# Performance work log

Hardware: AMD Instinct MI355X
Metric: run time of the kernel (lower is better)

The kernel has to match this reference:

```python
import jax, jax.numpy as jnp
import numpy as np
from jax import lax


def _edt(mask):
    """Exact Euclidean distance transform: for boolean mask [B,H,W], return the
    distance from each True pixel to the nearest False pixel (0 on False pixels).
    Two-phase separable algorithm:
      phase 1: 1D distance along axis H (rows) via forward/backward scans.
      phase 2: D2[i,j] = min_j' ( g[i,j']^2 + (j-j')^2 ) along axis W.
    """
    B, H, W = mask.shape
    BIG = jnp.float32(H + W)  # cap: larger than any in-image distance
    mT = jnp.transpose(mask, (1, 0, 2))  # [H,B,W] for scanning over rows

    def step(carry, m_row):
        d = jnp.where(m_row, jnp.minimum(carry + 1.0, BIG), 0.0)
        return d, d

    init = jnp.full((B, W), BIG, dtype=jnp.float32)
    _, fwd = lax.scan(step, init, mT)          # dist to nearest False above
    _, bwd = lax.scan(step, init, mT[::-1])    # dist to nearest False below
    g = jnp.minimum(fwd, bwd[::-1])            # [H,B,W] exact 1D vertical distance
    g2 = g * g

    j = jnp.arange(W, dtype=jnp.float32)
    sq = (j[:, None] - j[None, :]) ** 2        # [W(j), W(j')]
    # D2[h,b,j] = min_j' g2[h,b,j'] + (j-j')^2   (intermediate [H,B,W,W])
    D2 = jnp.min(g2[..., None, :] + sq, axis=-1)
    return jnp.sqrt(D2).transpose(1, 0, 2)     # [B,H,W]


def _dt(z):
    """Faithful port of the torch `dt`: fg-EDT + bg-EDT, zero if no foreground."""
    fg = z > 0.5
    f_dist = _edt(fg)        # distance from foreground pixels to background
    b_dist = _edt(~fg)       # distance from background pixels to foreground
    has_fg = jnp.any(fg, axis=(1, 2))[:, None, None]
    return jnp.where(has_fg, f_dist + b_dist, 0.0)


def setup_inputs() -> dict:
    key = jax.random.key(0)
    kx, ky = jax.random.split(key)
    x = jax.random.uniform(kx, (8, 256, 256), dtype=jnp.float32)
    y = jax.random.uniform(ky, (8, 256, 256), dtype=jnp.float32)
    return {"x": x, "y": y}


def reference(x, y):
    # distance transforms are computed on detached tensors in the original
    dt_x = lax.stop_gradient(_dt(x))
    dt_y = lax.stop_gradient(_dt(y))
    err = (x - y) ** 2
    dist = dt_x ** 2 + dt_y ** 2
    return jnp.mean(err * dist)
```

## Files before the change

kernel.cpp:

```cpp
#include <hip/hip_runtime.h>

#define BB 8
#define HH 256
#define WW 256
#define BHW (BB*HH*WW)
#define BIGV 512.0f


__global__ __launch_bounds__(256) void edt_vert(const float* __restrict__ x,
                                                const float* __restrict__ y,
                                                unsigned short* __restrict__ gdist,
                                                int* __restrict__ blkflag) {
    __shared__ float Cf[2][16][16];
    __shared__ float Cb[2][16][16];
    __shared__ int sAny;

    int blk = blockIdx.x;
    int tileIdx = blk & 15;
    int b  = (blk >> 4) & 7;
    int ip = blk >> 7;
    int t = threadIdx.x;
    int c = t & 15, s = t >> 4;

    if (t == 0) sAny = 0;

    const float* src = (ip ? y : x) + (size_t)b*HH*WW + tileIdx*16 + c;

    unsigned m = 0;
    const float* p = src + (size_t)(s*16)*WW;
    #pragma unroll
    for (int i = 0; i < 16; ++i) {
        if (p[(size_t)i*WW] > 0.5f) m |= (1u << i);
    }

    unsigned invm = (~m) & 0xFFFFu;
    Cf[0][s][c] = invm ? (float)(15 - (31 - __clz((int)invm))) : 1e9f;
    Cb[0][s][c] = invm ? (float)(__ffs((int)invm) - 1)          : 1e9f;
    Cf[1][s][c] = m    ? (float)(15 - (31 - __clz((int)m)))     : 1e9f;
    Cb[1][s][c] = m    ? (float)(__ffs((int)m) - 1)             : 1e9f;
    __syncthreads();
    if (m) sAny = 1;

    float e0 = BIGV, e1 = BIGV;
    #pragma unroll
    for (int sp = 0; sp < 15; ++sp) {
        float c0 = Cf[0][sp][c], c1 = Cf[1][sp][c];
        bool act = sp < s;
        e0 = act ? fminf(fminf(e0 + 16.0f, BIGV), c0) : e0;
        e1 = act ? fminf(fminf(e1 + 16.0f, BIGV), c1) : e1;
    }
    float f0 = BIGV, f1 = BIGV;
    #pragma unroll
    for (int sp = 15; sp >= 1; --sp) {
        float c0 = Cb[0][sp][c], c1 = Cb[1][sp][c];
        bool act = sp > s;
        f0 = act ? fminf(fminf(f0 + 16.0f, BIGV), c0) : f0;
        f1 = act ? fminf(fminf(f1 + 16.0f, BIGV), c1) : f1;
    }

    float b0v[16], b1v[16];
    float d0 = f0, d1 = f1;
    #pragma unroll
    for (int i = 15; i >= 0; --i) {
        bool bit = (m >> i) & 1u;
        d0 = !bit ? 0.0f : fminf(d0 + 1.0f, BIGV);
        d1 =  bit ? 0.0f : fminf(d1 + 1.0f, BIGV);
        b0v[i] = d0; b1v[i] = d1;
    }
    size_t base = (size_t)(ip*BB + b)*HH*WW + tileIdx*16 + c;
    d0 = e0; d1 = e1;
    #pragma unroll
    for (int i = 0; i < 16; ++i) {
        bool bit = (m >> i) & 1u;
        d0 = !bit ? 0.0f : fminf(d0 + 1.0f, BIGV);
        d1 =  bit ? 0.0f : fminf(d1 + 1.0f, BIGV);
        float g0 = fminf(d0, b0v[i]);
        float g1 = fminf(d1, b1v[i]);
        float gs = bit ? g0 : g1;
        gdist[base + (size_t)(s*16 + i)*WW] = (unsigned short)(int)gs;
    }

    __syncthreads();
    if (t == 0) blkflag[blk] = sAny;
}

__global__ __launch_bounds__(256) void row_pass(const float* __restrict__ x,
                                                const float* __restrict__ y,
                                                const unsigned short* __restrict__ gdist,
                                                const int* __restrict__ blkflag,
                                                float* __restrict__ partials) {
    __shared__ float sp0[768], sp1[768], sp2[768], sp3[768];
    __shared__ float wsum[4];
    __shared__ float sF[2];
    int bh = blockIdx.x;
    int b  = bh >> 8;
    int j  = threadIdx.x;
    size_t rowoff = (size_t)bh * WW;

    float xv = x[rowoff + j];
    float yv = y[rowoff + j];
    int gx = gdist[rowoff + j];
    int gy = gdist[(size_t)BHW + rowoff + j];
    bool mx = xv > 0.5f;
    bool my = yv > 0.5f;
    int gx2 = gx * gx, gy2 = gy * gy;
    float v0 = (float)(mx ? gx2 : 0);
    float v1 = (float)(mx ? 0 : gx2);
    float v2 = (float)(my ? gy2 : 0);
    float v3 = (float)(my ? 0 : gy2);

    sp0[j] = 1e9f; sp1[j] = 1e9f; sp2[j] = 1e9f; sp3[j] = 1e9f;
    sp0[j+512] = 1e9f; sp1[j+512] = 1e9f; sp2[j+512] = 1e9f; sp3[j+512] = 1e9f;
    sp0[j+256] = v0; sp1[j+256] = v1; sp2[j+256] = v2; sp3[j+256] = v3;

    if (j < 64) {
        int v = 0;
        if (j < 32) v = blkflag[((j < 16) ? 0 : 128) + b * 16 + (j & 15)];
        unsigned long long ball = __ballot(v != 0);
        if (j == 0) {
            sF[0] = (ball & 0xFFFFull) ? 1.0f : 0.0f;
            sF[1] = ((ball >> 16) & 0xFFFFull) ? 1.0f : 0.0f;
        }
    }
    __syncthreads();

    float b0 = v0, b1 = v1, b2 = v2, b3 = v3;
    for (int dl = 1; dl < 256; ++dl) {
        float d2 = (float)(dl * dl);
        float bmax = fmaxf(fmaxf(b0, b1), fmaxf(b2, b3));
        if (!__any(d2 < bmax)) break;
        int l = j + 256 - dl, r = j + 256 + dl;
        b0 = fminf(b0, fminf(d2 + sp0[l], d2 + sp0[r]));
        b1 = fminf(b1, fminf(d2 + sp1[l], d2 + sp1[r]));
        b2 = fminf(b2, fminf(d2 + sp2[l], d2 + sp2[r]));
        b3 = fminf(b3, fminf(d2 + sp3[l], d2 + sp3[r]));
    }

    float dtx = sF[0] != 0.0f ? (sqrtf(b0) + sqrtf(b1)) : 0.0f;
    float dty = sF[1] != 0.0f ? (sqrtf(b2) + sqrtf(b3)) : 0.0f;
    float e = xv - yv;
    float val = e * e * (dtx * dtx + dty * dty);

    for (int off = 32; off; off >>= 1) val += __shfl_down(val, off, 64);
    if ((j & 63) == 0) wsum[j >> 6] = val;
    __syncthreads();
    if (j == 0) partials[bh] = wsum[0] + wsum[1] + wsum[2] + wsum[3];
}

__global__ __launch_bounds__(256) void final_reduce(const float* __restrict__ partials,
                                                    float* __restrict__ out) {
    __shared__ float wsum[4];
    int j = threadIdx.x;
    float s = 0.0f;
    #pragma unroll
    for (int i = 0; i < 8; ++i) s += partials[i * 256 + j];
    for (int off = 32; off; off >>= 1) s += __shfl_down(s, off, 64);
    if ((j & 63) == 0) wsum[j >> 6] = s;
    __syncthreads();
    if (j == 0) out[0] = (wsum[0] + wsum[1] + wsum[2] + wsum[3]) * (1.0f / (float)BHW);
}

extern "C" void kernel_launch(void* const* d_in, const int* in_sizes, int n_in,
                              void* d_out, int out_size, void* d_ws, size_t ws_size,
                              hipStream_t stream) {
    const float* x = (const float*)d_in[0];
    const float* y = (const float*)d_in[1];
    float* out = (float*)d_out;

    char* ws = (char*)d_ws;
    unsigned short* gdist = (unsigned short*)ws;
    int* blkflag = (int*)(ws + (size_t)2 * BHW * sizeof(unsigned short));
    float* partials = (float*)(ws + (size_t)2 * BHW * sizeof(unsigned short) + 256 * sizeof(int));

    edt_vert<<<256, 256, 0, stream>>>(x, y, gdist, blkflag);
    row_pass<<<BB * HH, 256, 0, stream>>>(x, y, gdist, blkflag, partials);
    final_reduce<<<1, 256, 0, stream>>>(partials, out);
}
```

Baseline: 15.32 us.

## Merge row pass and final reduce into banded kernel with atomic accumulation

```diff
diff --git a/kernel.cpp b/kernel.cpp
--- a/kernel.cpp
+++ b/kernel.cpp
@@ -10,7 +10,8 @@
 __global__ __launch_bounds__(256) void edt_vert(const float* __restrict__ x,
                                                 const float* __restrict__ y,
                                                 unsigned short* __restrict__ gdist,
-                                                int* __restrict__ blkflag) {
+                                                int* __restrict__ blkflag,
+                                                float* __restrict__ out) {
     __shared__ float Cf[2][16][16];
     __shared__ float Cb[2][16][16];
     __shared__ int sAny;
@@ -23,6 +24,7 @@
     int c = t & 15, s = t >> 4;
 
     if (t == 0) sAny = 0;
+    if (blk == 0 && t == 0) out[0] = 0.0f;
 
     const float* src = (ip ? y : x) + (size_t)b*HH*WW + tileIdx*16 + c;
 
@@ -84,80 +86,83 @@
     if (t == 0) blkflag[blk] = sAny;
 }
 
-__global__ __launch_bounds__(256) void row_pass(const float* __restrict__ x,
-                                                const float* __restrict__ y,
-                                                const unsigned short* __restrict__ gdist,
-                                                const int* __restrict__ blkflag,
-                                                float* __restrict__ partials) {
-    __shared__ float sp0[768], sp1[768], sp2[768], sp3[768];
-    __shared__ float wsum[4];
+__global__ __launch_bounds__(1024) void row_band(const float* __restrict__ x,
+                                                 const float* __restrict__ y,
+                                                 const unsigned short* __restrict__ gdist,
+                                                 const int* __restrict__ blkflag,
+                                                 float* __restrict__ out) {
+    __shared__ float sp[4][4][768];
+    __shared__ float wsum[16];
     __shared__ float sF[2];
-    int bh = blockIdx.x;
-    int b  = bh >> 8;
-    int j  = threadIdx.x;
-    size_t rowoff = (size_t)bh * WW;
+    int blk = blockIdx.x;
+    int b    = blk >> 4;
+    int band = blk & 15;
+    int t = threadIdx.x;
+    int j  = t & 255;
+    int rs = t >> 8;
 
-    float xv = x[rowoff + j];
-    float yv = y[rowoff + j];
-    int gx = gdist[rowoff + j];
-    int gy = gdist[(size_t)BHW + rowoff + j];
-    bool mx = xv > 0.5f;
-    bool my = yv > 0.5f;
-    int gx2 = gx * gx, gy2 = gy * gy;
-    float v0 = (float)(mx ? gx2 : 0);
-    float v1 = (float)(mx ? 0 : gx2);
-    float v2 = (float)(my ? gy2 : 0);
-    float v3 = (float)(my ? 0 : gy2);
-
-    sp0[j] = 1e9f; sp1[j] = 1e9f; sp2[j] = 1e9f; sp3[j] = 1e9f;
-    sp0[j+512] = 1e9f; sp1[j+512] = 1e9f; sp2[j+512] = 1e9f; sp3[j+512] = 1e9f;
-    sp0[j+256] = v0; sp1[j+256] = v1; sp2[j+256] = v2; sp3[j+256] = v3;
-
-    if (j < 64) {
+    if (t < 64) {
         int v = 0;
-        if (j < 32) v = blkflag[((j < 16) ? 0 : 128) + b * 16 + (j & 15)];
+        if (t < 32) v = blkflag[((t < 16) ? 0 : 128) + b * 16 + (t & 15)];
         unsigned long long ball = __ballot(v != 0);
-        if (j == 0) {
+        if (t == 0) {
             sF[0] = (ball & 0xFFFFull) ? 1.0f : 0.0f;
             sF[1] = ((ball >> 16) & 0xFFFFull) ? 1.0f : 0.0f;
         }
     }
-    __syncthreads();
 
-    float b0 = v0, b1 = v1, b2 = v2, b3 = v3;
-    for (int dl = 1; dl < 256; ++dl) {
-        float d2 = (float)(dl * dl);
-        float bmax = fmaxf(fmaxf(b0, b1), fmaxf(b2, b3));
-        if (!__any(d2 < bmax)) break;
-        int l = j + 256 - dl, r = j + 256 + dl;
-        b0 = fminf(b0, fminf(d2 + sp0[l], d2 + sp0[r]));
-        b1 = fminf(b1, fminf(d2 + sp1[l], d2 + sp1[r]));
-        b2 = fminf(b2, fminf(d2 + sp2[l], d2 + sp2[r]));
-        b3 = fminf(b3, fminf(d2 + sp3[l], d2 + sp3[r]));
+    float acc = 0.0f;
+    #pragma unroll
+    for (int iter = 0; iter < 4; ++iter) {
+        int row = band * 16 + rs + iter * 4;
+        size_t rowoff = ((size_t)b * HH + row) * WW;
+
+        float xv = x[rowoff + j];
+        float yv = y[rowoff + j];
+        int gx = gdist[rowoff + j];
+        int gy = gdist[(size_t)BHW + rowoff + j];
+        bool mx = xv > 0.5f;
+        bool my = yv > 0.5f;
+        int gx2 = gx * gx, gy2 = gy * gy;
+        float v0 = (float)(mx ? gx2 : 0);
+        float v1 = (float)(mx ? 0 : gx2);
+        float v2 = (float)(my ? gy2 : 0);
+        float v3 = (float)(my ? 0 : gy2);
+
+        sp[rs][0][j] = 1e9f; sp[rs][1][j] = 1e9f; sp[rs][2][j] = 1e9f; sp[rs][3][j] = 1e9f;
+        sp[rs][0][j+512] = 1e9f; sp[rs][1][j+512] = 1e9f; sp[rs][2][j+512] = 1e9f; sp[rs][3][j+512] = 1e9f;
+        sp[rs][0][j+256] = v0; sp[rs][1][j+256] = v1; sp[rs][2][j+256] = v2; sp[rs][3][j+256] = v3;
+        __syncthreads();
+
+        float b0 = v0, b1 = v1, b2 = v2, b3 = v3;
+        for (int dl = 1; dl < 256; ++dl) {
+            float d2 = (float)(dl * dl);
+            float bmax = fmaxf(fmaxf(b0, b1), fmaxf(b2, b3));
+            if (!__any(d2 < bmax)) break;
+            int l = j + 256 - dl, r = j + 256 + dl;
+            b0 = fminf(b0, fminf(d2 + sp[rs][0][l], d2 + sp[rs][0][r]));
+            b1 = fminf(b1, fminf(d2 + sp[rs][1][l], d2 + sp[rs][1][r]));
+            b2 = fminf(b2, fminf(d2 + sp[rs][2][l], d2 + sp[rs][2][r]));
+            b3 = fminf(b3, fminf(d2 + sp[rs][3][l], d2 + sp[rs][3][r]));
+        }
+
+        float dtx = sF[0] != 0.0f ? (sqrtf(b0) + sqrtf(b1)) : 0.0f;
+        float dty = sF[1] != 0.0f ? (sqrtf(b2) + sqrtf(b3)) : 0.0f;
+        float e = xv - yv;
+        acc += e * e * (dtx * dtx + dty * dty);
+        __syncthreads();
     }
 
-    float dtx = sF[0] != 0.0f ? (sqrtf(b0) + sqrtf(b1)) : 0.0f;
-    float dty = sF[1] != 0.0f ? (sqrtf(b2) + sqrtf(b3)) : 0.0f;
-    float e = xv - yv;
-    float val = e * e * (dtx * dtx + dty * dty);
-
-    for (int off = 32; off; off >>= 1) val += __shfl_down(val, off, 64);
-    if ((j & 63) == 0) wsum[j >> 6] = val;
+    for (int off = 32; off; off >>= 1) acc += __shfl_down(acc, off, 64);
+    int wid = t >> 6, lane = t & 63;
+    if (lane == 0) wsum[wid] = acc;
     __syncthreads();
-    if (j == 0) partials[bh] = wsum[0] + wsum[1] + wsum[2] + wsum[3];
-}
-
-__global__ __launch_bounds__(256) void final_reduce(const float* __restrict__ partials,
-                                                    float* __restrict__ out) {
-    __shared__ float wsum[4];
-    int j = threadIdx.x;
-    float s = 0.0f;
-    #pragma unroll
-    for (int i = 0; i < 8; ++i) s += partials[i * 256 + j];
-    for (int off = 32; off; off >>= 1) s += __shfl_down(s, off, 64);
-    if ((j & 63) == 0) wsum[j >> 6] = s;
-    __syncthreads();
-    if (j == 0) out[0] = (wsum[0] + wsum[1] + wsum[2] + wsum[3]) * (1.0f / (float)BHW);
+    if (t == 0) {
+        float s = 0.0f;
+        #pragma unroll
+        for (int i = 0; i < 16; ++i) s += wsum[i];
+        atomicAdd(out, s * (1.0f / (float)BHW));
+    }
 }
 
 extern "C" void kernel_launch(void* const* d_in, const int* in_sizes, int n_in,
@@ -170,9 +175,7 @@
     char* ws = (char*)d_ws;
     unsigned short* gdist = (unsigned short*)ws;
     int* blkflag = (int*)(ws + (size_t)2 * BHW * sizeof(unsigned short));
-    float* partials = (float*)(ws + (size_t)2 * BHW * sizeof(unsigned short) + 256 * sizeof(int));
 
-    edt_vert<<<256, 256, 0, stream>>>(x, y, gdist, blkflag);
-    row_pass<<<BB * HH, 256, 0, stream>>>(x, y, gdist, blkflag, partials);
-    final_reduce<<<1, 256, 0, stream>>>(partials, out);
+    edt_vert<<<256, 256, 0, stream>>>(x, y, gdist, blkflag, out);
+    row_band<<<128, 1024, 0, stream>>>(x, y, gdist, blkflag, out);
 }
```

Measured after the change: 17.65 us. +15.2%, slower.
